# Kernel tuning notes

Measured on AMD Instinct MI355X. Metric: run time of the kernel, lower is better.

The kernel has to match this reference:

```python
import jax, jax.numpy as jnp
import numpy as np

SQ = 1.0 / np.sqrt(2.0)

def _haar_filters():
    dec_lo = np.array([SQ, SQ], np.float32); dec_hi = np.array([-SQ, SQ], np.float32)
    rec_lo = np.array([SQ, SQ], np.float32); rec_hi = np.array([SQ, -SQ], np.float32)
    def bank(lo, hi):
        ks = []
        for fz in (lo, hi):
            for fy in (lo, hi):
                for fx in (lo, hi):
                    ks.append(np.einsum('i,j,k->ijk', fz, fy, fx))
        return jnp.asarray(np.stack(ks, 0))  # [8,2,2,2]
    return bank(dec_lo, dec_hi), bank(rec_lo, rec_hi)

WT_F, IWT_F = _haar_filters()

def dwt3(x):
    # stride-2 2x2x2 cross-correlation == reshape + einsum (kernel size == stride)
    B, C, D, H, W = x.shape
    xr = x.reshape(B, C, D // 2, 2, H // 2, 2, W // 2, 2)
    return jnp.einsum('bcdzhywx,fzyx->bcfdhw', xr, WT_F)  # [B,C,8,D/2,H/2,W/2]

def idwt3(x):
    # conv_transpose3d stride 2 kernel 2: no overlap -> einsum + reshape
    B, C, _, D, H, W = x.shape
    out = jnp.einsum('bcfdhw,fzyx->bcdzhywx', x, IWT_F)
    return out.reshape(B, C, 2 * D, 2 * H, 2 * W)

def dwconv3(x, w, b=None):
    # depthwise 3x3x3 conv, padding SAME (torch padding='same', groups=C)
    y = jax.lax.conv_general_dilated(
        x, w, (1, 1, 1), 'SAME',
        dimension_numbers=('NCDHW', 'OIDHW', 'NCDHW'),
        feature_group_count=x.shape[1])
    if b is not None:
        y = y + b[None, :, None, None, None]
    return y

WT_LEVELS = 2

def setup_inputs() -> dict:
    key = jax.random.key(0)
    ks = jax.random.split(key, 6)
    B, C, D, H, W = 1, 64, 64, 64, 64
    return {
        'x': jax.random.normal(ks[0], (B, C, D, H, W), jnp.float32),
        'base_w': jax.random.normal(ks[1], (C, 1, 3, 3, 3), jnp.float32) * 0.1,
        'base_b': jax.random.normal(ks[2], (C,), jnp.float32) * 0.02,
        'base_scale_w': jnp.ones((1, C, 1, 1, 1), jnp.float32),
        'wconv_w0': jax.random.normal(ks[3], (C * 8, 1, 3, 3, 3), jnp.float32) * 0.1,
        'wconv_w1': jax.random.normal(ks[4], (C * 8, 1, 3, 3, 3), jnp.float32) * 0.1,
        'wscale0': jnp.full((1, C * 8, 1, 1, 1), 0.1, jnp.float32),
        'wscale1': jnp.full((1, C * 8, 1, 1, 1), 0.1, jnp.float32),
        'lambd': jnp.float32(0.05),
    }

def reference(x, base_w, base_b, base_scale_w, wconv_w0, wconv_w1, wscale0, wscale1, lambd):
    wconv_ws = (wconv_w0, wconv_w1)
    wscales = (wscale0, wscale1)
    lls, hfs, shapes = [], [], []
    cur = x
    for i in range(WT_LEVELS):
        shapes.append(cur.shape)
        pd, ph, pw = cur.shape[2] % 2, cur.shape[3] % 2, cur.shape[4] % 2
        if pd or ph or pw:
            cur = jnp.pad(cur, ((0, 0), (0, 0), (0, pd), (0, ph), (0, pw)))
        cx = dwt3(cur)                     # [B,C,8,d,h,w]
        cur = cx[:, :, 0]                  # LL passes to next level
        B, C, _, d, h, w = cx.shape
        t = dwconv3(cx.reshape(B, C * 8, d, h, w), wconv_ws[i])
        t = t.reshape(B, C, 8, d, h, w)
        ll, hf = t[:, :, :1], t[:, :, 1:]
        hf = jnp.sign(hf) * jax.nn.relu(jnp.abs(hf) - lambd)  # soft threshold
        t = jnp.concatenate([ll, hf], axis=2)
        t = (t.reshape(B, C * 8, d, h, w) * wscales[i]).reshape(B, C, 8, d, h, w)
        lls.append(t[:, :, 0]); hfs.append(t[:, :, 1:])
    nxt = jnp.float32(0.0)
    for i in range(WT_LEVELS - 1, -1, -1):
        cll = lls[i] + nxt
        cx = jnp.concatenate([cll[:, :, None], hfs[i]], axis=2)
        nxt = idwt3(cx)
        sh = shapes[i]
        nxt = nxt[:, :, :sh[2], :sh[3], :sh[4]]
    base = dwconv3(x, base_w, base_b) * base_scale_w
    return base + nxt
```

## Files before the change

### kernel.cpp

```cpp
#include <hip/hip_runtime.h>

#define SQ3F 0.35355339059327379f

__device__ __forceinline__ void haar_fwd(const float v[8], float o[8]) {
    float ax[8];
#pragma unroll
    for (int i = 0; i < 4; ++i) {
        float a = v[2 * i], b = v[2 * i + 1];
        ax[2 * i]     = a + b;
        ax[2 * i + 1] = b - a;
    }
    float ay[8];
#pragma unroll
    for (int z = 0; z < 2; ++z)
#pragma unroll
        for (int bx = 0; bx < 2; ++bx) {
            float a = ax[z * 4 + bx], b = ax[z * 4 + 2 + bx];
            ay[z * 4 + bx]     = a + b;
            ay[z * 4 + 2 + bx] = b - a;
        }
#pragma unroll
    for (int j = 0; j < 4; ++j) {
        float a = ay[j], b = ay[4 + j];
        o[j]     = (a + b) * SQ3F;
        o[4 + j] = (b - a) * SQ3F;
    }
}

__device__ __forceinline__ void haar_inv(const float t[8], float o[8]) {
    float az[8];
#pragma unroll
    for (int j = 0; j < 4; ++j) {
        float lo = t[j], hi = t[4 + j];
        az[j]     = lo + hi;
        az[4 + j] = lo - hi;
    }
    float ay[8];
#pragma unroll
    for (int z = 0; z < 2; ++z)
#pragma unroll
        for (int bx = 0; bx < 2; ++bx) {
            float lo = az[z * 4 + bx], hi = az[z * 4 + 2 + bx];
            ay[z * 4 + bx]     = lo + hi;
            ay[z * 4 + 2 + bx] = lo - hi;
        }
#pragma unroll
    for (int i = 0; i < 4; ++i) {
        float lo = ay[2 * i], hi = ay[2 * i + 1];
        o[2 * i]     = (lo + hi) * SQ3F;
        o[2 * i + 1] = (lo - hi) * SQ3F;
    }
}

template <int SO>
__global__ __launch_bounds__(256) void dwt3_k(const float* __restrict__ in,
                                              int inChStride,
                                              float* __restrict__ out) {
    constexpr int SI = SO * 2;
    int idx = blockIdx.x * 256 + threadIdx.x;
    int w = idx % SO;
    int h = (idx / SO) % SO;
    int d = (idx / (SO * SO)) % SO;
    int c = idx / (SO * SO * SO);
    const float* ip = in + (long)c * inChStride;
    float v[8];
#pragma unroll
    for (int z = 0; z < 2; ++z)
#pragma unroll
        for (int y = 0; y < 2; ++y) {
            const float2 p =
                *(const float2*)(ip + ((2 * d + z) * SI + (2 * h + y)) * SI + 2 * w);
            v[z * 4 + y * 2]     = p.x;
            v[z * 4 + y * 2 + 1] = p.y;
        }
    float o[8];
    haar_fwd(v, o);
    int s = (d * SO + h) * SO + w;
#pragma unroll
    for (int f = 0; f < 8; ++f) out[(c * 8 + f) * (SO * SO * SO) + s] = o[f];
}

template <int S, int PH>
__device__ __forceinline__ void conv_step(const float* __restrict__ ip, int zo,
                                          int ty, int x0,
                                          const float* __restrict__ wv,
                                          float win[3][3][6], float lam, float sc,
                                          bool hf, float* __restrict__ op) {
    constexpr int sPrev = (PH + 2) % 3;
    constexpr int sCur  = PH;
    constexpr int sNext = (PH + 1) % 3;
    {
        int zz = zo + 1;
        bool zok = zz < S;
        const float* pp = ip + zz * S * S;
#pragma unroll
        for (int dy = 0; dy < 3; ++dy) {
            int yy  = ty - 1 + dy;
            bool yok = zok && ((unsigned)yy < (unsigned)S);
            const float* rp = pp + yy * S;
            win[sNext][dy][0] = (yok && x0 > 0) ? rp[x0 - 1] : 0.f;
            float4 m = yok ? *(const float4*)(rp + x0) : float4{0.f, 0.f, 0.f, 0.f};
            win[sNext][dy][1] = m.x;
            win[sNext][dy][2] = m.y;
            win[sNext][dy][3] = m.z;
            win[sNext][dy][4] = m.w;
            win[sNext][dy][5] = (yok && (x0 + 4 < S)) ? rp[x0 + 4] : 0.f;
        }
    }
    float acc[4] = {0.f, 0.f, 0.f, 0.f};
#pragma unroll
    for (int dz = 0; dz < 3; ++dz) {
        const float(*wp)[6] = (dz == 0) ? win[sPrev] : (dz == 1) ? win[sCur] : win[sNext];
#pragma unroll
        for (int dy = 0; dy < 3; ++dy)
#pragma unroll
            for (int dx = 0; dx < 3; ++dx) {
                float wgt = wv[dz * 9 + dy * 3 + dx];
#pragma unroll
                for (int j = 0; j < 4; ++j) acc[j] += wp[dy][dx + j] * wgt;
            }
    }
    float4 r;
    float* rr = (float*)&r;
#pragma unroll
    for (int j = 0; j < 4; ++j) {
        float t = acc[j];
        if (hf) {
            float a = fabsf(t) - lam;
            t       = a > 0.f ? copysignf(a, t) : 0.f;
        }
        rr[j] = t * sc;
    }
    *(float4*)(op + (zo * S + ty) * S + x0) = r;
}

template <int S, int CPB>
__global__ __launch_bounds__(256) void dwconv_soft_roll_k(
    const float* __restrict__ in, const float* __restrict__ wt,
    const float* __restrict__ wscale, const float* __restrict__ lambd_p,
    float* __restrict__ out) {
    constexpr int TX = S / 4;
    int tid = threadIdx.x;
    int tx  = tid % TX;
    int ty  = (tid / TX) % S;
    int cs  = tid / (TX * S);
    int cc  = blockIdx.x * CPB + cs;
    const float* ip = in + (long)cc * (S * S * S);
    float* op       = out + (long)cc * (S * S * S);
    float wv[27];
#pragma unroll
    for (int k = 0; k < 27; ++k) wv[k] = wt[cc * 27 + k];
    float lam = *lambd_p;
    float sc  = wscale[cc];
    bool hf   = (cc & 7) != 0;
    int x0    = 4 * tx;

    float win[3][3][6];
#pragma unroll
    for (int a = 0; a < 3; ++a)
#pragma unroll
        for (int b = 0; b < 3; ++b)
#pragma unroll
            for (int k = 0; k < 6; ++k) win[a][b][k] = 0.f;
    {
#pragma unroll
        for (int dy = 0; dy < 3; ++dy) {
            int yy  = ty - 1 + dy;
            bool yok = (unsigned)yy < (unsigned)S;
            const float* rp = ip + yy * S;
            win[0][dy][0] = (yok && x0 > 0) ? rp[x0 - 1] : 0.f;
            float4 m = yok ? *(const float4*)(rp + x0) : float4{0.f, 0.f, 0.f, 0.f};
            win[0][dy][1] = m.x;
            win[0][dy][2] = m.y;
            win[0][dy][3] = m.z;
            win[0][dy][4] = m.w;
            win[0][dy][5] = (yok && (x0 + 4 < S)) ? rp[x0 + 4] : 0.f;
        }
    }
#pragma unroll 1
    for (int zb = 0; zb < S; zb += 3) {
        conv_step<S, 0>(ip, zb, ty, x0, wv, win, lam, sc, hf, op);
        if (zb + 1 < S) conv_step<S, 1>(ip, zb + 1, ty, x0, wv, win, lam, sc, hf, op);
        if (zb + 2 < S) conv_step<S, 2>(ip, zb + 2, ty, x0, wv, win, lam, sc, hf, op);
    }
}

template <int SI>
__global__ __launch_bounds__(256) void idwt_add_k(const float* __restrict__ t,
                                                  float* __restrict__ dst,
                                                  int dstChStride) {
    int idx = blockIdx.x * 256 + threadIdx.x;
    int w = idx % SI, h = (idx / SI) % SI, d = (idx / (SI * SI)) % SI,
        c = idx / (SI * SI * SI);
    int s = (d * SI + h) * SI + w;
    float tf[8], o[8];
#pragma unroll
    for (int f = 0; f < 8; ++f) tf[f] = t[(c * 8 + f) * (SI * SI * SI) + s];
    haar_inv(tf, o);
    float* dp = dst + (long)c * dstChStride;
    constexpr int SD = SI * 2;
#pragma unroll
    for (int z = 0; z < 2; ++z)
#pragma unroll
        for (int y = 0; y < 2; ++y) {
            float* q = dp + ((2 * d + z) * SD + (2 * h + y)) * SD + 2 * w;
            q[0] += o[z * 4 + y * 2];
            q[1] += o[z * 4 + y * 2 + 1];
        }
}

__global__ __launch_bounds__(256) void final_cube_k(const float* __restrict__ x,
                                                    const float* __restrict__ t0,
                                                    const float* __restrict__ bw,
                                                    const float* __restrict__ bb,
                                                    const float* __restrict__ bscale,
                                                    float* __restrict__ out) {
    int c    = blockIdx.x >> 7;
    int cell = ((blockIdx.x & 127) << 8) + threadIdx.x;
    int w = cell & 31, h = (cell >> 5) & 31, d = cell >> 10;

    float tf[8];
#pragma unroll
    for (int f = 0; f < 8; ++f) tf[f] = t0[((c * 8 + f) << 15) + cell];
    float contrib[8];
    haar_inv(tf, contrib);

    const float* wp0 = bw + c * 27;
    float wv[27];
#pragma unroll
    for (int k = 0; k < 27; ++k) wv[k] = wp0[k];
    float bias = bb[c], scl = bscale[c];

    const float* ip = x + ((long)c << 18);
    float p[4][4][4];
#pragma unroll
    for (int pz = 0; pz < 4; ++pz) {
        int zz  = 2 * d - 1 + pz;
        bool zok = (unsigned)zz < 64u;
#pragma unroll
        for (int py = 0; py < 4; ++py) {
            int yy  = 2 * h - 1 + py;
            bool yok = zok && ((unsigned)yy < 64u);
            const float* rp = ip + ((zz << 6) + yy) * 64;
#pragma unroll
            for (int px = 0; px < 4; ++px) {
                int xx = 2 * w - 1 + px;
                bool ok = yok && ((unsigned)xx < 64u);
                p[pz][py][px] = ok ? rp[xx] : 0.f;
            }
        }
    }
#pragma unroll
    for (int oz = 0; oz < 2; ++oz)
#pragma unroll
        for (int oy = 0; oy < 2; ++oy) {
            float r[2];
#pragma unroll
            for (int ox = 0; ox < 2; ++ox) {
                float acc = 0.f;
#pragma unroll
                for (int kz = 0; kz < 3; ++kz)
#pragma unroll
                    for (int ky = 0; ky < 3; ++ky)
#pragma unroll
                        for (int kx = 0; kx < 3; ++kx)
                            acc += p[oz + kz][oy + ky][ox + kx] * wv[kz * 9 + ky * 3 + kx];
                r[ox] = (acc + bias) * scl + contrib[oz * 4 + oy * 2 + ox];
            }
            *(float2*)(out + (((c << 6) + 2 * d + oz) * 64 + 2 * h + oy) * 64 + 2 * w) =
                float2{r[0], r[1]};
        }
}

extern "C" void kernel_launch(void* const* d_in, const int* in_sizes, int n_in,
                              void* d_out, int out_size, void* d_ws, size_t ws_size,
                              hipStream_t stream) {
    const float* x      = (const float*)d_in[0];
    const float* base_w = (const float*)d_in[1];
    const float* base_b = (const float*)d_in[2];
    const float* base_s = (const float*)d_in[3];
    const float* w0     = (const float*)d_in[4];
    const float* w1     = (const float*)d_in[5];
    const float* ws0    = (const float*)d_in[6];
    const float* ws1    = (const float*)d_in[7];
    const float* lambd  = (const float*)d_in[8];
    float* out = (float*)d_out;

    float* cx0 = (float*)d_ws;
    float* t0  = cx0 + 16777216;
    float* cx1 = t0 + 16777216;
    float* t1  = cx1 + 2097152;

    dwt3_k<32><<<8192, 256, 0, stream>>>(x, 262144, cx0);
    dwconv_soft_roll_k<32, 1><<<512, 256, 0, stream>>>(cx0, w0, ws0, lambd, t0);
    dwt3_k<16><<<1024, 256, 0, stream>>>(cx0, 8 * 32768, cx1);
    dwconv_soft_roll_k<16, 4><<<128, 256, 0, stream>>>(cx1, w1, ws1, lambd, t1);
    idwt_add_k<16><<<1024, 256, 0, stream>>>(t1, t0, 8 * 32768);
    final_cube_k<<<8192, 256, 0, stream>>>(x, t0, base_w, base_b, base_s, out);
}
```

Measured before the change: 254.0 us.

## Fuse level-0 DWT with depthwise conv and tile final base conv in LDS

Replaces the separate level-0 DWT and its depthwise conv with one kernel. It computes Haar coefficients plane by plane into a rolling three-plane shared buffer and runs the 3x3x3 conv plus soft threshold directly, writing only the LL band for the next level. This removes the full 8-band cx0 round trip through global memory. The final kernel also stages an x halo tile in LDS instead of doing 64 scattered global loads per thread. In exchange, each x element is reloaded by both band-half blocks and the fused kernel adds more syncs and lower occupancy.

```diff
diff --git a/kernel.cpp b/kernel.cpp
--- a/kernel.cpp
+++ b/kernel.cpp
@@ -49,6 +49,116 @@
         float lo = ay[2 * i], hi = ay[2 * i + 1];
         o[2 * i]     = (lo + hi) * SQ3F;
         o[2 * i + 1] = (lo - hi) * SQ3F;
+    }
+}
+
+#define L0_PAD 34
+__global__ __launch_bounds__(512, 2) void fused_l0_k(
+    const float* __restrict__ x, const float* __restrict__ wt,
+    const float* __restrict__ wscale, const float* __restrict__ lambd_p,
+    float* __restrict__ t0, float* __restrict__ ll) {
+    __shared__ float bp[3][4][32][L0_PAD];
+    int bx   = blockIdx.x;
+    int bh   = bx & 1;
+    int slab = (bx >> 1) & 3;
+    int c    = bx >> 3;
+    int z0   = slab * 8;
+    int tid  = threadIdx.x;
+
+    for (int i = tid; i < 3 * 4 * 32; i += 512) {
+        float* row = &bp[0][0][0][0] + i * L0_PAD;
+        row[0]  = 0.f;
+        row[33] = 0.f;
+    }
+
+    int fl   = tid >> 7;
+    int f    = __builtin_amdgcn_readfirstlane(bh * 4 + fl);
+    int u    = tid & 127;
+    int cty  = u >> 2;
+    int cx0i = (u & 3) * 8;
+    int cc   = c * 8 + f;
+    float wv[27];
+    const float* wp = wt + cc * 27;
+#pragma unroll
+    for (int k = 0; k < 27; ++k) wv[k] = wp[k];
+    float lam = *lambd_p;
+    float sc  = wscale[cc];
+    bool hf   = (f != 0);
+
+    const float* xc = x + ((long)c << 18);
+
+    auto compute_plane = [&](int p, int slot) {
+#pragma unroll
+        for (int cell2 = 0; cell2 < 2; ++cell2) {
+            int cell = tid + cell2 * 512;
+            int y = cell >> 5, xx = cell & 31;
+            float v[8];
+            bool ok = (unsigned)p < 32u;
+            if (ok) {
+#pragma unroll
+                for (int z = 0; z < 2; ++z)
+#pragma unroll
+                    for (int yy = 0; yy < 2; ++yy) {
+                        float2 q = *(const float2*)(xc + (((2 * p + z) << 6) +
+                                                          (2 * y + yy)) * 64 + 2 * xx);
+                        v[z * 4 + yy * 2]     = q.x;
+                        v[z * 4 + yy * 2 + 1] = q.y;
+                    }
+            } else {
+#pragma unroll
+                for (int k = 0; k < 8; ++k) v[k] = 0.f;
+            }
+            float o[8];
+            haar_fwd(v, o);
+#pragma unroll
+            for (int k = 0; k < 4; ++k) bp[slot][k][y][xx + 1] = o[bh * 4 + k];
+            if (bh == 0 && ok && (unsigned)(p - z0) < 8u)
+                ll[(c << 15) + (p << 10) + cell] = o[0];
+        }
+    };
+
+    compute_plane(z0 - 1, (z0 + 2) % 3);
+    compute_plane(z0, z0 % 3);
+    __syncthreads();
+
+    for (int zb = z0; zb < z0 + 8; ++zb) {
+        compute_plane(zb + 1, (zb + 1) % 3);
+        __syncthreads();
+
+        float acc[8] = {0.f, 0.f, 0.f, 0.f, 0.f, 0.f, 0.f, 0.f};
+#pragma unroll
+        for (int dz = 0; dz < 3; ++dz) {
+            int slot = (zb + 2 + dz) % 3;
+#pragma unroll
+            for (int dy = 0; dy < 3; ++dy) {
+                int yy = cty - 1 + dy;
+                if ((unsigned)yy < 32u) {
+                    float r[10];
+#pragma unroll
+                    for (int k = 0; k < 10; ++k) r[k] = bp[slot][fl][yy][cx0i + k];
+#pragma unroll
+                    for (int dx = 0; dx < 3; ++dx) {
+                        float wgt = wv[dz * 9 + dy * 3 + dx];
+#pragma unroll
+                        for (int j = 0; j < 8; ++j) acc[j] += r[dx + j] * wgt;
+                    }
+                }
+            }
+        }
+        float res[8];
+#pragma unroll
+        for (int j = 0; j < 8; ++j) {
+            float t = acc[j];
+            if (hf) {
+                float a = fabsf(t) - lam;
+                t       = a > 0.f ? copysignf(a, t) : 0.f;
+            }
+            res[j] = t * sc;
+        }
+        float* op = t0 + ((long)cc << 15) + (zb << 10) + cty * 32 + cx0i;
+        *(float4*)(op)     = float4{res[0], res[1], res[2], res[3]};
+        *(float4*)(op + 4) = float4{res[4], res[5], res[6], res[7]};
+        __syncthreads();
     }
 }
 
@@ -209,15 +319,38 @@
         }
 }
 
-__global__ __launch_bounds__(256) void final_cube_k(const float* __restrict__ x,
+__global__ __launch_bounds__(256) void final_tile_k(const float* __restrict__ x,
                                                     const float* __restrict__ t0,
                                                     const float* __restrict__ bw,
                                                     const float* __restrict__ bb,
                                                     const float* __restrict__ bscale,
                                                     float* __restrict__ out) {
-    int c    = blockIdx.x >> 7;
-    int cell = ((blockIdx.x & 127) << 8) + threadIdx.x;
-    int w = cell & 31, h = (cell >> 5) & 31, d = cell >> 10;
+    __shared__ float xs[10 * 18 * 18];
+    int bx  = blockIdx.x;
+    int c   = bx >> 7;
+    int rem = bx & 127;
+    int dt = rem >> 4, ht = (rem >> 2) & 3, wtl = rem & 3;
+    int zb = 8 * dt - 1, yb = 16 * ht - 1, xbg = 16 * wtl - 1;
+    const float* xc = x + ((long)c << 18);
+    for (int i = threadIdx.x; i < 3240; i += 256) {
+        int pz = i / 324;
+        int r  = i - pz * 324;
+        int py = r / 18;
+        int px = r - py * 18;
+        int zg = zb + pz, yg = yb + py, xg = xbg + px;
+        bool ok = ((unsigned)zg < 64u) && ((unsigned)yg < 64u) && ((unsigned)xg < 64u);
+        xs[i] = ok ? xc[((zg << 6) + yg) * 64 + xg] : 0.f;
+    }
+    const float* wp0 = bw + c * 27;
+    float wv[27];
+#pragma unroll
+    for (int k = 0; k < 27; ++k) wv[k] = wp0[k];
+    float bias = bb[c], scl = bscale[c];
+    __syncthreads();
+
+    int tw = threadIdx.x & 7, th = (threadIdx.x >> 3) & 7, td = threadIdx.x >> 6;
+    int d = dt * 4 + td, h = ht * 8 + th, w = wtl * 8 + tw;
+    int cell = (d << 10) + (h << 5) + w;
 
     float tf[8];
 #pragma unroll
@@ -225,36 +358,21 @@
     float contrib[8];
     haar_inv(tf, contrib);
 
-    const float* wp0 = bw + c * 27;
-    float wv[27];
-#pragma unroll
-    for (int k = 0; k < 27; ++k) wv[k] = wp0[k];
-    float bias = bb[c], scl = bscale[c];
-
-    const float* ip = x + ((long)c << 18);
     float p[4][4][4];
 #pragma unroll
-    for (int pz = 0; pz < 4; ++pz) {
-        int zz  = 2 * d - 1 + pz;
-        bool zok = (unsigned)zz < 64u;
-#pragma unroll
-        for (int py = 0; py < 4; ++py) {
-            int yy  = 2 * h - 1 + py;
-            bool yok = zok && ((unsigned)yy < 64u);
-            const float* rp = ip + ((zz << 6) + yy) * 64;
-#pragma unroll
-            for (int px = 0; px < 4; ++px) {
-                int xx = 2 * w - 1 + px;
-                bool ok = yok && ((unsigned)xx < 64u);
-                p[pz][py][px] = ok ? rp[xx] : 0.f;
-            }
-        }
-    }
+    for (int pz = 0; pz < 4; ++pz)
+#pragma unroll
+        for (int py = 0; py < 4; ++py)
+#pragma unroll
+            for (int px = 0; px < 4; ++px)
+                p[pz][py][px] =
+                    xs[(2 * td + pz) * 324 + (2 * th + py) * 18 + 2 * tw + px];
+
 #pragma unroll
     for (int oz = 0; oz < 2; ++oz)
 #pragma unroll
         for (int oy = 0; oy < 2; ++oy) {
-            float r[2];
+            float r2[2];
 #pragma unroll
             for (int ox = 0; ox < 2; ++ox) {
                 float acc = 0.f;
@@ -265,10 +383,10 @@
 #pragma unroll
                         for (int kx = 0; kx < 3; ++kx)
                             acc += p[oz + kz][oy + ky][ox + kx] * wv[kz * 9 + ky * 3 + kx];
-                r[ox] = (acc + bias) * scl + contrib[oz * 4 + oy * 2 + ox];
+                r2[ox] = (acc + bias) * scl + contrib[oz * 4 + oy * 2 + ox];
             }
             *(float2*)(out + (((c << 6) + 2 * d + oz) * 64 + 2 * h + oy) * 64 + 2 * w) =
-                float2{r[0], r[1]};
+                float2{r2[0], r2[1]};
         }
 }
 
@@ -286,15 +404,14 @@
     const float* lambd  = (const float*)d_in[8];
     float* out = (float*)d_out;
 
-    float* cx0 = (float*)d_ws;
-    float* t0  = cx0 + 16777216;
+    float* ll  = (float*)d_ws;
+    float* t0  = ll + 2097152;
     float* cx1 = t0 + 16777216;
     float* t1  = cx1 + 2097152;
 
-    dwt3_k<32><<<8192, 256, 0, stream>>>(x, 262144, cx0);
-    dwconv_soft_roll_k<32, 1><<<512, 256, 0, stream>>>(cx0, w0, ws0, lambd, t0);
-    dwt3_k<16><<<1024, 256, 0, stream>>>(cx0, 8 * 32768, cx1);
+    fused_l0_k<<<512, 512, 0, stream>>>(x, w0, ws0, lambd, t0, ll);
+    dwt3_k<16><<<1024, 256, 0, stream>>>(ll, 32768, cx1);
     dwconv_soft_roll_k<16, 4><<<128, 256, 0, stream>>>(cx1, w1, ws1, lambd, t1);
     idwt_add_k<16><<<1024, 256, 0, stream>>>(t1, t0, 8 * 32768);
-    final_cube_k<<<8192, 256, 0, stream>>>(x, t0, base_w, base_b, base_s, out);
-}
+    final_tile_k<<<8192, 256, 0, stream>>>(x, t0, base_w, base_b, base_s, out);
+}
```

Result: slower. 289.5 us (+14.0%).
